# Optimization experiments

Hardware: AMD Instinct MI355X
Metric: run time of the kernel (lower is better)

## Reference

```python
import jax, jax.numpy as jnp
import numpy as np

N_CELLS = 196608  # 12 * 4**7 (HEALPix zoom 7)
NH = 9            # cell + 8 neighbors
F_IN = 64
F_OUT = 64


def setup_inputs() -> dict:
    key = jax.random.key(0)
    k1, k2, k3 = jax.random.split(key, 3)
    x = jax.random.normal(k1, (1, 1, 1, N_CELLS, F_IN), dtype=jnp.float32)
    adjc = jax.random.randint(k2, (N_CELLS, NH), 0, N_CELLS, dtype=jnp.int32)
    W = jax.random.normal(k3, (NH * F_IN, F_OUT), dtype=jnp.float32) * (1.0 / np.sqrt(NH * F_IN))
    return {"x": x, "adjc": adjc, "W": W}


def reference(x, adjc, W):
    # get_nh: gather neighborhood features along the cell axis.
    # x: [B, V, T, N, F], adjc: [N, NH] -> xnh: [B, V, T, N, NH, F]
    xnh = jnp.take(x, adjc, axis=3)
    B, V, T, N = xnh.shape[:4]
    # LinearLayer: flatten (NH, F) -> NH*F, dense projection to F_OUT (no bias)
    xf = xnh.reshape(B, V, T, N, NH * x.shape[-1])
    out = jnp.einsum('bvtnk,ko->bvtno', xf, W)  # [B, V, T, N, F_OUT]
    return out
```

## Files before the change

kernel.cpp:

```cpp
#include <hip/hip_runtime.h>
#include <hip/hip_bf16.h>
#include <stdint.h>

#define N_CELLS 196608
#define NH 9
#define F 64
#define K_TOT (NH * F)
#define K_STEPS (K_TOT / 32)
#define NFRAG (K_STEPS * 4)
#define WLDS_SHORTS (NFRAG * 64 * 8)
#define BLOCK 512

typedef __attribute__((ext_vector_type(8))) short bf16x8;
typedef __attribute__((ext_vector_type(4))) float f32x4;

__device__ inline unsigned short f2bf(float f) {
    union { float f; uint32_t u; } v; v.f = f;
    uint32_t u = v.u;
    uint32_t r = u + 0x7FFFu + ((u >> 16) & 1u);
    return (unsigned short)(r >> 16);
}

__global__ __launch_bounds__(256) void convert_x_i8(
        const float* __restrict__ x, signed char* __restrict__ xq,
        float* __restrict__ stab) {
    int gid = blockIdx.x * blockDim.x + threadIdx.x;
    int row = gid >> 4;
    int k   = (gid & 15) * 4;
    f32x4 v = *reinterpret_cast<const f32x4*>(x + (size_t)row * F + k);
    float m = fmaxf(fmaxf(fabsf(v[0]), fabsf(v[1])),
                    fmaxf(fabsf(v[2]), fabsf(v[3])));
    #pragma unroll
    for (int d = 1; d < 16; d <<= 1) m = fmaxf(m, __shfl_xor(m, d, 64));
    float s  = m * (1.0f / 127.0f);
    float rs = (m > 0.f) ? 127.0f / m : 0.f;
    int p = (((k & 31) >> 3) << 4) + ((k >> 5) << 3) + (k & 7);
    unsigned int d = 0;
    #pragma unroll
    for (int q = 0; q < 4; ++q) {
        int qi = (int)rintf(v[q] * rs);
        d |= ((unsigned int)(qi & 0xff)) << (q * 8);
    }
    *reinterpret_cast<unsigned int*>(xq + (size_t)row * F + p) = d;
    if ((gid & 15) == 0) stab[row] = s;
}

__global__ __launch_bounds__(256) void convert_w_kernel(
        const float* __restrict__ W, unsigned short* __restrict__ wb) {
    int tid = blockIdx.x * blockDim.x + threadIdx.x;
    int l = tid & 63;
    int frag = tid >> 6;
    int kk = frag >> 2, t = frag & 3;
    int k0 = kk * 32 + (l >> 4) * 8;
    int o  = t * 16 + (l & 15);
    unsigned short tmp[8];
    #pragma unroll
    for (int j = 0; j < 8; ++j) tmp[j] = f2bf(W[(size_t)(k0 + j) * F + o]);
    *reinterpret_cast<bf16x8*>(wb + (size_t)tid * 8) =
        *reinterpret_cast<const bf16x8*>(tmp);
}

__global__ __launch_bounds__(BLOCK, 2) void fused_gather_gemm_v9(
        const signed char* __restrict__ xq, const float* __restrict__ stab,
        const int* __restrict__ adjc, const unsigned short* __restrict__ wb,
        float* __restrict__ out) {
    __shared__ unsigned short wlds[WLDS_SHORTS];

    const int wave = threadIdx.x >> 6;
    const int lane = threadIdx.x & 63;
    const int lo = lane & 15, hi = lane >> 4;
    const int wcell = blockIdx.x * 256 + wave * 32;

    int   idx[2][NH];
    float sc[2][NH];
    #pragma unroll
    for (int m = 0; m < 2; ++m) {
        const int* ap = adjc + (size_t)(wcell + m * 16 + lo) * NH;
        #pragma unroll
        for (int j = 0; j < NH; ++j) idx[m][j] = __builtin_nontemporal_load(ap + j);
        #pragma unroll
        for (int j = 0; j < NH; ++j) sc[m][j] = stab[idx[m][j]];
    }

    auto loadA = [&](int m, int j) -> uint4 {
        return *reinterpret_cast<const uint4*>(
                xq + (size_t)idx[m][j] * F + hi * 16);
    };
    auto expand = [&](unsigned int d0, unsigned int d1, float s) -> bf16x8 {
        unsigned short tmp[8];
        #pragma unroll
        for (int q = 0; q < 8; ++q) {
            unsigned int dw = (q < 4) ? d0 : d1;
            int c = (int)(signed char)((dw >> ((q & 3) * 8)) & 0xff);
            tmp[q] = f2bf((float)c * s);
        }
        return *reinterpret_cast<const bf16x8*>(tmp);
    };

    {
        const bf16x8* src = reinterpret_cast<const bf16x8*>(wb);
        bf16x8* dst = reinterpret_cast<bf16x8*>(wlds);
        #pragma unroll
        for (int it = 0; it < 9; ++it)
            dst[it * BLOCK + threadIdx.x] = src[it * BLOCK + threadIdx.x];
    }

    uint4 aS[3][2];
    #pragma unroll
    for (int m = 0; m < 2; ++m) {
        aS[0][m] = loadA(m, 0);
        aS[1][m] = loadA(m, 1);
    }
    __syncthreads();

    f32x4 acc[2][4];
    #pragma unroll
    for (int m = 0; m < 2; ++m)
        #pragma unroll
        for (int t = 0; t < 4; ++t) acc[m][t] = f32x4{0.f, 0.f, 0.f, 0.f};

    #pragma unroll
    for (int j = 0; j < NH; ++j) {
        const int cur = j % 3;
        const int nxt = (j + 2) % 3;
        if (j + 2 < NH) {
            #pragma unroll
            for (int m = 0; m < 2; ++m) aS[nxt][m] = loadA(m, j + 2);
        }
        __builtin_amdgcn_sched_barrier(0);
        #pragma unroll
        for (int h = 0; h < 2; ++h) {
            bf16x8 a[2];
            #pragma unroll
            for (int m = 0; m < 2; ++m) {
                unsigned int d0 = h ? aS[cur][m].z : aS[cur][m].x;
                unsigned int d1 = h ? aS[cur][m].w : aS[cur][m].y;
                a[m] = expand(d0, d1, sc[m][j]);
            }
            const int kk = j * 2 + h;
            #pragma unroll
            for (int t = 0; t < 4; ++t) {
                bf16x8 b = *reinterpret_cast<const bf16x8*>(
                        &wlds[((size_t)(kk * 4 + t) * 64 + lane) * 8]);
                #pragma unroll
                for (int m = 0; m < 2; ++m)
                    acc[m][t] = __builtin_amdgcn_mfma_f32_16x16x32_bf16(
                            a[m], b, acc[m][t], 0, 0, 0);
            }
        }
        __builtin_amdgcn_sched_barrier(0);
    }

    __syncthreads();
    float* ldsf = reinterpret_cast<float*>(wlds);
    const int rbase = wave * 2048;
    #pragma unroll
    for (int m = 0; m < 2; ++m)
        #pragma unroll
        for (int t = 0; t < 4; ++t)
            #pragma unroll
            for (int r = 0; r < 4; ++r)
                ldsf[rbase + (m * 16 + hi * 4 + r) * 64 + t * 16 + lo] =
                        acc[m][t][r];
    __syncthreads();
    #pragma unroll
    for (int p = 0; p < 8; ++p) {
        const int f = p * 256 + lane * 4;
        f32x4 v = *reinterpret_cast<const f32x4*>(&ldsf[rbase + f]);
        *reinterpret_cast<f32x4*>(&out[(size_t)wcell * F + f]) = v;
    }
}

__global__ void naive_kernel(const float* __restrict__ x,
                             const int* __restrict__ adjc,
                             const float* __restrict__ W,
                             float* __restrict__ out) {
    int n = blockIdx.x;
    int o = threadIdx.x;
    float acc = 0.f;
    for (int j = 0; j < NH; ++j) {
        int idx = adjc[(size_t)n * NH + j];
        for (int f = 0; f < F; ++f)
            acc += x[(size_t)idx * F + f] * W[(size_t)(j * F + f) * F + o];
    }
    out[(size_t)n * F + o] = acc;
}

extern "C" void kernel_launch(void* const* d_in, const int* in_sizes, int n_in,
                              void* d_out, int out_size, void* d_ws, size_t ws_size,
                              hipStream_t stream) {
    const float* x    = (const float*)d_in[0];
    const int*   adjc = (const int*)d_in[1];
    const float* W    = (const float*)d_in[2];
    float* out = (float*)d_out;

    const size_t need_xq = (size_t)N_CELLS * F;
    const size_t need_s  = (size_t)N_CELLS * sizeof(float);
    const size_t need_w  = (size_t)K_TOT * F * sizeof(unsigned short);

    if (ws_size >= need_xq + need_s + need_w) {
        signed char*    xq   = (signed char*)d_ws;
        float*          stab = (float*)((char*)d_ws + need_xq);
        unsigned short* wb   = (unsigned short*)((char*)d_ws + need_xq + need_s);
        convert_x_i8<<<(N_CELLS * 16) / 256, 256, 0, stream>>>(x, xq, stab);
        convert_w_kernel<<<(K_STEPS * 4 * 64) / 256, 256, 0, stream>>>(W, wb);
        fused_gather_gemm_v9<<<N_CELLS / 256, BLOCK, 0, stream>>>(
                xq, stab, adjc, wb, out);
    } else {
        naive_kernel<<<N_CELLS, F, 0, stream>>>(x, adjc, W, out);
    }
}
```

Baseline: 64.74 us.

## Switch gather-GEMM to int8 MFMA with per-column int8 weight quantization

Weights are now quantized to int8 with per-output-column scales, and the gathered int8 activations feed 16x16x64 i8 MFMA directly. Per-neighbor row scales are applied to the integer partial products, and the column scales are applied at the epilogue. This removes the per-element int8-to-bf16 expansion ALU work and halves the LDS weight footprint. In exchange it adds weight quantization error on top of the existing activation quantization, an extra small prep kernel, and scalar FMA rescaling per MFMA.

```diff
diff --git a/kernel.cpp b/kernel.cpp
--- a/kernel.cpp
+++ b/kernel.cpp
@@ -6,20 +6,13 @@
 #define NH 9
 #define F 64
 #define K_TOT (NH * F)
-#define K_STEPS (K_TOT / 32)
-#define NFRAG (K_STEPS * 4)
-#define WLDS_SHORTS (NFRAG * 64 * 8)
 #define BLOCK 512
-
-typedef __attribute__((ext_vector_type(8))) short bf16x8;
+#define NFRAG (NH * 4)
+#define WQ_BYTES (NFRAG * 64 * 16)
+#define LDS_BYTES 65536
+
+typedef __attribute__((ext_vector_type(4))) int   i32x4;
 typedef __attribute__((ext_vector_type(4))) float f32x4;
-
-__device__ inline unsigned short f2bf(float f) {
-    union { float f; uint32_t u; } v; v.f = f;
-    uint32_t u = v.u;
-    uint32_t r = u + 0x7FFFu + ((u >> 16) & 1u);
-    return (unsigned short)(r >> 16);
-}
 
 __global__ __launch_bounds__(256) void convert_x_i8(
         const float* __restrict__ x, signed char* __restrict__ xq,
@@ -32,39 +25,62 @@
                     fmaxf(fabsf(v[2]), fabsf(v[3])));
     #pragma unroll
     for (int d = 1; d < 16; d <<= 1) m = fmaxf(m, __shfl_xor(m, d, 64));
-    float s  = m * (1.0f / 127.0f);
     float rs = (m > 0.f) ? 127.0f / m : 0.f;
-    int p = (((k & 31) >> 3) << 4) + ((k >> 5) << 3) + (k & 7);
     unsigned int d = 0;
     #pragma unroll
     for (int q = 0; q < 4; ++q) {
         int qi = (int)rintf(v[q] * rs);
         d |= ((unsigned int)(qi & 0xff)) << (q * 8);
     }
-    *reinterpret_cast<unsigned int*>(xq + (size_t)row * F + p) = d;
-    if ((gid & 15) == 0) stab[row] = s;
-}
-
-__global__ __launch_bounds__(256) void convert_w_kernel(
-        const float* __restrict__ W, unsigned short* __restrict__ wb) {
-    int tid = blockIdx.x * blockDim.x + threadIdx.x;
-    int l = tid & 63;
-    int frag = tid >> 6;
-    int kk = frag >> 2, t = frag & 3;
-    int k0 = kk * 32 + (l >> 4) * 8;
-    int o  = t * 16 + (l & 15);
-    unsigned short tmp[8];
-    #pragma unroll
-    for (int j = 0; j < 8; ++j) tmp[j] = f2bf(W[(size_t)(k0 + j) * F + o]);
-    *reinterpret_cast<bf16x8*>(wb + (size_t)tid * 8) =
-        *reinterpret_cast<const bf16x8*>(tmp);
-}
-
-__global__ __launch_bounds__(BLOCK, 2) void fused_gather_gemm_v9(
+    *reinterpret_cast<unsigned int*>(xq + (size_t)row * F + k) = d;
+    if ((gid & 15) == 0) stab[row] = m * (1.0f / 127.0f);
+}
+
+__global__ __launch_bounds__(256) void convert_wscale(
+        const float* __restrict__ W, float* __restrict__ wscale) {
+    __shared__ float mx[64];
+    int o = threadIdx.x & 63, chunk = threadIdx.x >> 6;
+    if (threadIdx.x < 64) mx[threadIdx.x] = 0.f;
+    __syncthreads();
+    float m = 0.f;
+    for (int k = chunk * 144; k < (chunk + 1) * 144; ++k)
+        m = fmaxf(m, fabsf(W[(size_t)k * F + o]));
+    atomicMax(reinterpret_cast<int*>(&mx[o]), __float_as_int(m));
+    __syncthreads();
+    if (threadIdx.x < 64) wscale[threadIdx.x] = mx[threadIdx.x] * (1.0f / 127.0f);
+}
+
+__global__ __launch_bounds__(256) void convert_wq(
+        const float* __restrict__ W, const float* __restrict__ wscale,
+        unsigned char* __restrict__ wq) {
+    int gid = blockIdx.x * blockDim.x + threadIdx.x;
+    int l = gid & 63, fid = gid >> 6;
+    int j = fid >> 2, t = fid & 3;
+    int hi = l >> 4, lo = l & 15;
+    int o = t * 16 + lo;
+    float ws = wscale[o];
+    float inv = (ws > 0.f) ? 1.0f / ws : 0.f;
+    unsigned int dw[4];
+    #pragma unroll
+    for (int w = 0; w < 4; ++w) {
+        unsigned int d = 0;
+        #pragma unroll
+        for (int b = 0; b < 4; ++b) {
+            int k = j * 64 + hi * 16 + w * 4 + b;
+            int qi = (int)rintf(W[(size_t)k * F + o] * inv);
+            d |= ((unsigned int)(qi & 0xff)) << (b * 8);
+        }
+        dw[w] = d;
+    }
+    *reinterpret_cast<uint4*>(wq + (size_t)gid * 16) =
+        make_uint4(dw[0], dw[1], dw[2], dw[3]);
+}
+
+__global__ __launch_bounds__(BLOCK, 2) void fused_gather_gemm_v10(
         const signed char* __restrict__ xq, const float* __restrict__ stab,
-        const int* __restrict__ adjc, const unsigned short* __restrict__ wb,
-        float* __restrict__ out) {
-    __shared__ unsigned short wlds[WLDS_SHORTS];
+        const int* __restrict__ adjc, const unsigned char* __restrict__ wq,
+        const float* __restrict__ wscale, float* __restrict__ out) {
+    __shared__ __align__(16) unsigned char lds[LDS_BYTES];
 
     const int wave = threadIdx.x >> 6;
     const int lane = threadIdx.x & 63;
@@ -82,30 +98,22 @@
         for (int j = 0; j < NH; ++j) sc[m][j] = stab[idx[m][j]];
     }
 
-    auto loadA = [&](int m, int j) -> uint4 {
-        return *reinterpret_cast<const uint4*>(
+    auto loadA = [&](int m, int j) -> i32x4 {
+        return *reinterpret_cast<const i32x4*>(
                 xq + (size_t)idx[m][j] * F + hi * 16);
     };
-    auto expand = [&](unsigned int d0, unsigned int d1, float s) -> bf16x8 {
-        unsigned short tmp[8];
-        #pragma unroll
-        for (int q = 0; q < 8; ++q) {
-            unsigned int dw = (q < 4) ? d0 : d1;
-            int c = (int)(signed char)((dw >> ((q & 3) * 8)) & 0xff);
-            tmp[q] = f2bf((float)c * s);
-        }
-        return *reinterpret_cast<const bf16x8*>(tmp);
-    };
 
     {
-        const bf16x8* src = reinterpret_cast<const bf16x8*>(wb);
-        bf16x8* dst = reinterpret_cast<bf16x8*>(wlds);
-        #pragma unroll
-        for (int it = 0; it < 9; ++it)
-            dst[it * BLOCK + threadIdx.x] = src[it * BLOCK + threadIdx.x];
-    }
-
-    uint4 aS[3][2];
+        const i32x4* src = reinterpret_cast<const i32x4*>(wq);
+        i32x4* dst = reinterpret_cast<i32x4*>(lds);
+        #pragma unroll
+        for (int it = 0; it < 5; ++it) {
+            int i = it * BLOCK + threadIdx.x;
+            if (i < NFRAG * 64) dst[i] = src[i];
+        }
+    }
+
+    i32x4 aS[3][2];
     #pragma unroll
     for (int m = 0; m < 2; ++m) {
         aS[0][m] = loadA(m, 0);
@@ -118,6 +126,9 @@
     for (int m = 0; m < 2; ++m)
         #pragma unroll
         for (int t = 0; t < 4; ++t) acc[m][t] = f32x4{0.f, 0.f, 0.f, 0.f};
+
+    const i32x4* wl = reinterpret_cast<const i32x4*>(lds);
+    const int sbase = (lane >> 4) * 20;
 
     #pragma unroll
     for (int j = 0; j < NH; ++j) {
@@ -128,31 +139,36 @@
             for (int m = 0; m < 2; ++m) aS[nxt][m] = loadA(m, j + 2);
         }
         __builtin_amdgcn_sched_barrier(0);
-        #pragma unroll
-        for (int h = 0; h < 2; ++h) {
-            bf16x8 a[2];
+
+        float sd[2][4];
+        #pragma unroll
+        for (int m = 0; m < 2; ++m)
+            #pragma unroll
+            for (int r = 0; r < 4; ++r)
+                sd[m][r] = __shfl(sc[m][j], sbase + r, 64);
+
+        #pragma unroll
+        for (int t = 0; t < 4; ++t) {
+            i32x4 b = wl[(j * 4 + t) * 64 + lane];
             #pragma unroll
             for (int m = 0; m < 2; ++m) {
-                unsigned int d0 = h ? aS[cur][m].z : aS[cur][m].x;
-                unsigned int d1 = h ? aS[cur][m].w : aS[cur][m].y;
-                a[m] = expand(d0, d1, sc[m][j]);
+                i32x4 iz = {0, 0, 0, 0};
+                i32x4 iacc = __builtin_amdgcn_mfma_i32_16x16x64_i8(
+                        aS[cur][m], b, iz, 0, 0, 0);
+                #pragma unroll
+                for (int r = 0; r < 4; ++r)
+                    acc[m][t][r] += sd[m][r] * (float)iacc[r];
             }
-            const int kk = j * 2 + h;
-            #pragma unroll
-            for (int t = 0; t < 4; ++t) {
-                bf16x8 b = *reinterpret_cast<const bf16x8*>(
-                        &wlds[((size_t)(kk * 4 + t) * 64 + lane) * 8]);
-                #pragma unroll
-                for (int m = 0; m < 2; ++m)
-                    acc[m][t] = __builtin_amdgcn_mfma_f32_16x16x32_bf16(
-                            a[m], b, acc[m][t], 0, 0, 0);
-            }
         }
         __builtin_amdgcn_sched_barrier(0);
     }
 
-    __syncthreads();
-    float* ldsf = reinterpret_cast<float*>(wlds);
+    float wsc[4];
+    #pragma unroll
+    for (int t = 0; t < 4; ++t) wsc[t] = wscale[t * 16 + lo];
+
+    __syncthreads();
+    float* ldsf = reinterpret_cast<float*>(lds);
     const int rbase = wave * 2048;
     #pragma unroll
     for (int m = 0; m < 2; ++m)
@@ -161,7 +177,7 @@
             #pragma unroll
             for (int r = 0; r < 4; ++r)
                 ldsf[rbase + (m * 16 + hi * 4 + r) * 64 + t * 16 + lo] =
-                        acc[m][t][r];
+                        acc[m][t][r] * wsc[t];
     __syncthreads();
     #pragma unroll
     for (int p = 0; p < 8; ++p) {
@@ -196,16 +212,19 @@
 
     const size_t need_xq = (size_t)N_CELLS * F;
     const size_t need_s  = (size_t)N_CELLS * sizeof(float);
-    const size_t need_w  = (size_t)K_TOT * F * sizeof(unsigned short);
-
-    if (ws_size >= need_xq + need_s + need_w) {
-        signed char*    xq   = (signed char*)d_ws;
-        float*          stab = (float*)((char*)d_ws + need_xq);
-        unsigned short* wb   = (unsigned short*)((char*)d_ws + need_xq + need_s);
-        convert_x_i8<<<(N_CELLS * 16) / 256, 256, 0, stream>>>(x, xq, stab);
-        convert_w_kernel<<<(K_STEPS * 4 * 64) / 256, 256, 0, stream>>>(W, wb);
-        fused_gather_gemm_v9<<<N_CELLS / 256, BLOCK, 0, stream>>>(
-                xq, stab, adjc, wb, out);
+    const size_t need_wq = WQ_BYTES;
+    const size_t need_ws = 64 * sizeof(float);
+
+    if (ws_size >= need_xq + need_s + need_wq + need_ws) {
+        signed char*   xq  = (signed char*)d_ws;
+        float*         st  = (float*)((char*)d_ws + need_xq);
+        unsigned char* wqp = (unsigned char*)((char*)d_ws + need_xq + need_s);
+        float*         wsp = (float*)((char*)d_ws + need_xq + need_s + need_wq);
+        convert_x_i8<<<(N_CELLS * 16) / 256, 256, 0, stream>>>(x, xq, st);
+        convert_wscale<<<1, 256, 0, stream>>>(W, wsp);
+        convert_wq<<<(NFRAG * 64) / 256, 256, 0, stream>>>(W, wsp, wqp);
+        fused_gather_gemm_v10<<<N_CELLS / 256, BLOCK, 0, stream>>>(
+                xq, st, adjc, wqp, wsp, out);
     } else {
         naive_kernel<<<N_CELLS, F, 0, stream>>>(x, adjc, W, out);
     }
```

Result: slower. 145.0 us (+123.9%).
